# Optimization experiments

Measured on AMD Instinct MI355X. Metric: run time of the kernel, lower is better.

Reference implementation:

```python
import jax, jax.numpy as jnp
import numpy as np
import math

SQRT32 = math.sqrt(32.0)


def _l2norm(x, eps=1e-12):
    # matches torch.nn.functional.normalize(dim=-1): x / max(||x||, eps)
    n = jnp.linalg.norm(x, axis=-1, keepdims=True)
    return x / jnp.maximum(n, eps)


def setup_inputs() -> dict:
    key = jax.random.key(0)
    k1, k2 = jax.random.split(key)
    z = jax.random.normal(k1, (8, 256, 32, 32), dtype=jnp.float32)
    # trunc_normal_(std=0.02) init approximated by scaled normal
    embed_weight = jax.random.normal(k2, (16384, 256), dtype=jnp.float32) * 0.02
    return {"z": z, "embed_weight": embed_weight}


def reference(z, embed_weight):
    # z: [b, d, h, w] channel-first -> pack to [b*h*w, d]
    b, d, h, w = z.shape
    zf = jnp.transpose(z, (0, 2, 3, 1)).reshape(-1, d)  # [N, d]

    # l2_norm=True, no predefined codebook: distance = -z @ normalize(E)^T
    ew = _l2norm(embed_weight)                          # [K, d]
    dist = -(zf @ ew.T)                                 # [N, K]
    min_encoding_indices = jnp.argmin(dist, axis=1)     # [N]

    # gather UNnormalized embedding rows, then normalize (as in source)
    z_q = _l2norm(embed_weight[min_encoding_indices])   # [N, d]

    # straight-through estimator
    z_q = zf + jax.lax.stop_gradient(z_q - zf)

    loss = jnp.zeros((1,), dtype=z.dtype)

    # unpack to [b, h, w, d]
    zq_bhwd = z_q.reshape(b, h, w, d)
    # torch .long() truncates toward zero; astype(int) does the same
    bit_indices = (zq_bhwd * SQRT32).astype(jnp.int32) + 4
    zq_out = jnp.transpose(zq_bhwd, (0, 3, 1, 2))       # [b, d, h, w]

    return zq_out, min_encoding_indices, bit_indices, loss
```

## Files before the change

### kernel.cpp

```cpp
#include <hip/hip_runtime.h>
#include <math.h>

#define D      256
#define K      16384
#define NPTS   8192
#define DELTA  0.2f
#define LCAP   1024
#define MAXCAP 4000000u

#define O_IDX  2097152
#define O_BIT  2105344
#define O_LOSS 4202496

typedef __attribute__((ext_vector_type(8))) short bf16x8;
typedef __attribute__((ext_vector_type(4))) float f32x4;
typedef unsigned long long u64;

__device__ __forceinline__ unsigned f2s(float f) {
    unsigned u = __float_as_uint(f);
    return (u & 0x80000000u) ? ~u : (u | 0x80000000u);
}
__device__ __forceinline__ float s2f(unsigned s) {
    return __uint_as_float((s & 0x80000000u) ? (s & 0x7fffffffu) : ~s);
}
__device__ __forceinline__ unsigned short f2bf(float f) {
    unsigned u = __float_as_uint(f);
    u += 0x7fffu + ((u >> 16) & 1u);
    return (unsigned short)(u >> 16);
}


__global__ __launch_bounds__(256) void prep(const float* __restrict__ E,
                                            const float* __restrict__ z,
                                            float* __restrict__ den,
                                            unsigned short* __restrict__ ewbT,
                                            unsigned short* __restrict__ zfbT,
                                            float* __restrict__ zf32,
                                            unsigned* __restrict__ gmax,
                                            u64* __restrict__ keys,
                                            unsigned* __restrict__ cnt) {
    const int blk = blockIdx.x, tid = threadIdx.x;
    if (blk < 512) {
        const int lane = tid & 63, wave = tid >> 6;
        if (blk < 32)        gmax[blk * 256 + tid] = 0u;
        else if (blk < 64)   keys[(blk - 32) * 256 + tid] = 0ull;
        else if (blk == 64 && tid < 2) cnt[tid] = 0u;
        #pragma unroll
        for (int j = 0; j < 8; ++j) {
            const int row = blk * 32 + wave * 8 + j;
            const float4 v = *(const float4*)(E + (size_t)row * D + lane * 4);
            float ss = v.x * v.x + v.y * v.y + v.z * v.z + v.w * v.w;
            #pragma unroll
            for (int o = 1; o < 64; o <<= 1) ss += __shfl_xor(ss, o);
            const float dn = fmaxf(sqrtf(ss), 1e-12f);
            const unsigned lo = (unsigned)f2bf(v.x / dn) | ((unsigned)f2bf(v.y / dn) << 16);
            const unsigned hi = (unsigned)f2bf(v.z / dn) | ((unsigned)f2bf(v.w / dn) << 16);
            *(uint2*)(ewbT + ((size_t)(lane >> 1) * K + row) * 8 + (lane & 1) * 4)
                = make_uint2(lo, hi);
            if (lane == 0) den[row] = dn;
        }
    } else {
        const int bi = blk - 512;
        const int b = bi >> 4, hw0 = (bi & 15) * 64;
        __shared__ float t[64][65];
        for (int dc = 0; dc < D; dc += 64) {
            #pragma unroll
            for (int it = 0; it < 16; ++it) {
                const int idx = it * 256 + tid;
                const int dl = idx >> 6, hw = idx & 63;
                t[dl][hw] = z[(size_t)(b * 256 + dc + dl) * 1024 + hw0 + hw];
            }
            __syncthreads();
            #pragma unroll
            for (int it = 0; it < 16; ++it) {
                const int idx = it * 256 + tid;
                const int pl = idx >> 6, dl = idx & 63;
                const float v = t[dl][pl];
                const int p = b * 1024 + hw0 + pl, k = dc + dl;
                zfbT[((size_t)(k >> 3) * NPTS + p) * 8 + (k & 7)] = f2bf(v);
                zf32[(size_t)p * D + k] = v;
            }
            __syncthreads();
        }
    }
}

#define GEMM_CORE()                                                                 \
    f32x4 acc[4][4];                                                                \
    _Pragma("unroll")                                                               \
    for (int i = 0; i < 4; ++i)                                                     \
        _Pragma("unroll")                                                           \
        for (int j = 0; j < 4; ++j) acc[i][j] = (f32x4){0.f, 0.f, 0.f, 0.f};        \
    {                                                                               \
        const unsigned short* pA = zfbT + ((size_t)quad * NPTS + m0 + wm * 64 + col) * 8; \
        const unsigned short* pB = ewbT + ((size_t)quad * K    + n0 + wn * 64 + col) * 8; \
        _Pragma("unroll")                                                           \
        for (int dc = 0; dc < 8; ++dc) {                                            \
            bf16x8 af[4], bfr[4];                                                   \
            _Pragma("unroll")                                                       \
            for (int mt = 0; mt < 4; ++mt)                                          \
                af[mt] = *(const bf16x8*)(pA + (size_t)dc * 4 * NPTS * 8 + mt * 128);\
            _Pragma("unroll")                                                       \
            for (int nt = 0; nt < 4; ++nt)                                          \
                bfr[nt] = *(const bf16x8*)(pB + (size_t)dc * 4 * K * 8 + nt * 128); \
            _Pragma("unroll")                                                       \
            for (int mt = 0; mt < 4; ++mt)                                          \
                _Pragma("unroll")                                                   \
                for (int nt = 0; nt < 4; ++nt)                                      \
                    acc[mt][nt] = __builtin_amdgcn_mfma_f32_16x16x32_bf16(af[mt], bfr[nt], \
                                                                          acc[mt][nt], 0, 0, 0); \
        }                                                                           \
    }

__global__ __launch_bounds__(256, 3) void score_seed(const unsigned short* __restrict__ zfbT,
                                                     const unsigned short* __restrict__ ewbT,
                                                     unsigned* __restrict__ gmax,
                                                     u64* __restrict__ cand,
                                                     unsigned* __restrict__ cnt,
                                                     unsigned cap) {
    __shared__ unsigned thrS[128];
    __shared__ u64 lbuf[LCAP];
    __shared__ unsigned lcount, lbase;

    const int tid = threadIdx.x, lane = tid & 63, wave = tid >> 6;
    const int quad = lane >> 4, col = lane & 15;
    const int wm = wave >> 1, wn = wave & 1;
    const int m0 = blockIdx.x * 128;
    const int n0 = blockIdx.y * 128;
    const int shsrc = lane & 48;

    if (tid < 128) thrS[tid] = 0u;
    if (tid == 0) lcount = 0u;

    GEMM_CORE()
    __syncthreads();

    float red[4][4];
    #pragma unroll
    for (int mt = 0; mt < 4; ++mt)
        #pragma unroll
        for (int r = 0; r < 4; ++r)
            red[mt][r] = fmaxf(fmaxf(acc[mt][0][r], acc[mt][1][r]),
                               fmaxf(acc[mt][2][r], acc[mt][3][r]));
    #pragma unroll
    for (int off = 1; off < 16; off <<= 1)
        #pragma unroll
        for (int mt = 0; mt < 4; ++mt)
            #pragma unroll
            for (int r = 0; r < 4; ++r)
                red[mt][r] = fmaxf(red[mt][r], __shfl_xor(red[mt][r], off));
    #pragma unroll
    for (int mt = 0; mt < 4; ++mt)
        #pragma unroll
        for (int r = 0; r < 4; ++r) {
            const int pl = wm * 64 + mt * 16 + quad * 4 + r;
            unsigned cur = 0;
            if (col == 0) {
                const unsigned enc = f2s(red[mt][r]);
                const unsigned old = atomicMax(&thrS[pl], enc);
                cur = old > enc ? old : enc;
            }
            cur = (unsigned)__shfl((int)cur, shsrc);
            red[mt][r] = s2f(cur) - DELTA;
        }

    const int ncode0 = n0 + wn * 64 + col;
    #pragma unroll
    for (int mt = 0; mt < 4; ++mt) {
        #pragma unroll
        for (int r = 0; r < 4; ++r) {
            const float tp = red[mt][r];
            const unsigned pt = m0 + wm * 64 + mt * 16 + quad * 4 + r;
            #pragma unroll
            for (int nt = 0; nt < 4; ++nt) {
                const float v = acc[mt][nt][r];
                if (v >= tp) {
                    const unsigned slot = atomicAdd(&lcount, 1u);
                    const u64 e = ((u64)((pt << 14) | (unsigned)(ncode0 + nt * 16)) << 32)
                                  | f2s(v);
                    if (slot < LCAP) lbuf[slot] = e;
                    else {
                        const unsigned g = atomicAdd(cnt, 1u);
                        if (g < cap) cand[g] = e;
                    }
                }
            }
        }
    }

    __syncthreads();
    if (tid < 128) atomicMax(&gmax[m0 + tid], thrS[tid]);
    const unsigned m_ = lcount < LCAP ? lcount : LCAP;
    if (tid == 0) lbase = atomicAdd(cnt, m_);
    __syncthreads();
    for (unsigned i = tid; i < m_; i += 256) {
        const unsigned g = lbase + i;
        if (g < cap) cand[g] = lbuf[i];
    }
}

__global__ __launch_bounds__(256, 3) void score_main(const unsigned short* __restrict__ zfbT,
                                                     const unsigned short* __restrict__ ewbT,
                                                     const unsigned* __restrict__ gmax,
                                                     u64* __restrict__ cand,
                                                     unsigned* __restrict__ cnt,
                                                     unsigned cap) {
    __shared__ float thrL[128];
    __shared__ u64 lbuf[LCAP];
    __shared__ unsigned lcount, lbase;

    const int tid = threadIdx.x, lane = tid & 63, wave = tid >> 6;
    const int quad = lane >> 4, col = lane & 15;
    const int wm = wave >> 1, wn = wave & 1;
    const int m0 = blockIdx.x * 128;
    const int n0 = (16 + blockIdx.y) * 128;

    if (tid < 128) thrL[tid] = s2f(gmax[m0 + tid]) - DELTA;
    if (tid == 0) lcount = 0u;

    GEMM_CORE()
    __syncthreads();

    const int ncode0 = n0 + wn * 64 + col;
    #pragma unroll
    for (int mt = 0; mt < 4; ++mt) {
        #pragma unroll
        for (int r = 0; r < 4; ++r) {
            const int pl = wm * 64 + mt * 16 + quad * 4 + r;
            const float tp = thrL[pl];
            #pragma unroll
            for (int nt = 0; nt < 4; ++nt) {
                const float v = acc[mt][nt][r];
                if (v >= tp) {
                    const unsigned slot = atomicAdd(&lcount, 1u);
                    const u64 e = ((u64)(((unsigned)pl + m0) << 14 | (unsigned)(ncode0 + nt * 16)) << 32)
                                  | f2s(v);
                    if (slot < LCAP) lbuf[slot] = e;
                    else {
                        const unsigned g = atomicAdd(cnt, 1u);
                        if (g < cap) cand[g] = e;
                    }
                }
            }
        }
    }

    __syncthreads();
    const unsigned m_ = lcount < LCAP ? lcount : LCAP;
    if (tid == 0) lbase = atomicAdd(cnt, m_);
    __syncthreads();
    for (unsigned i = tid; i < m_; i += 256) {
        const unsigned g = lbase + i;
        if (g < cap) cand[g] = lbuf[i];
    }
}

__global__ __launch_bounds__(256) void cand_max(const u64* __restrict__ cand,
                                                const unsigned* __restrict__ cnt,
                                                unsigned* __restrict__ gmax,
                                                unsigned cap) {
    const unsigned total = min(cnt[0], cap);
    const unsigned stride = gridDim.x * 256;
    for (unsigned i = blockIdx.x * 256 + threadIdx.x; i < total; i += stride) {
        const u64 e = cand[i];
        atomicMax(&gmax[(unsigned)(e >> 46)], (unsigned)(e & 0xffffffffull));
    }
}

__global__ __launch_bounds__(256) void rescore(const float* __restrict__ zf32,
                                               const float* __restrict__ E,
                                               const float* __restrict__ den,
                                               const unsigned* __restrict__ gmax,
                                               const u64* __restrict__ cand,
                                               const unsigned* __restrict__ cnt,
                                               u64* __restrict__ keys,
                                               unsigned cap) {
    const unsigned total = min(cnt[0], cap);
    const int lane = threadIdx.x & 63;
    const unsigned w = (blockIdx.x * 256 + threadIdx.x) >> 6;
    const unsigned nw = gridDim.x * 4;
    for (unsigned base = w * 64; base < total; base += nw * 64) {
        const unsigned i = base + lane;
        u64 e = 0;
        bool keep = false;
        if (i < total) {
            e = cand[i];
            const int p = (int)(e >> 46);
            keep = (s2f((unsigned)(e & 0xffffffffull)) >= s2f(gmax[p]) - DELTA);
        }
        u64 mask = __ballot(keep);
        while (mask) {
            const int src = __ffsll((long long)mask) - 1;
            mask &= mask - 1;
            const unsigned pc = (unsigned)__shfl((int)(unsigned)(e >> 32), src);
            const int p = pc >> 14, c = pc & 16383;
            const float dinv = 1.0f / den[c];
            const float4 a = *(const float4*)(zf32 + (size_t)p * D + lane * 4);
            const float4 b = *(const float4*)(E + (size_t)c * D + lane * 4);
            float sv = fmaf(a.x, b.x * dinv, fmaf(a.y, b.y * dinv,
                       fmaf(a.z, b.z * dinv, a.w * (b.w * dinv))));
            #pragma unroll
            for (int o = 1; o < 64; o <<= 1) sv += __shfl_xor(sv, o);
            if (lane == 0)
                atomicMax(keys + p, ((u64)f2s(sv) << 32) | (unsigned)(16383 - c));
        }
    }
}

__global__ __launch_bounds__(256) void finalize(const float* __restrict__ E,
                                                const float* __restrict__ den,
                                                const u64* __restrict__ keys,
                                                float* __restrict__ out) {
    __shared__ float t[32][257];
    __shared__ int sIdx[32];
    __shared__ float sDen[32];
    const int tid = threadIdx.x;
    const int n0 = blockIdx.x * 32;
    if (tid < 32) {
        const u64 key = keys[n0 + tid];
        const int idx = 16383 - (int)(unsigned)(key & 0xffffffffull);
        sIdx[tid] = idx;
        sDen[tid] = den[idx];
        out[O_IDX + n0 + tid] = (float)idx;
    }
    __syncthreads();
    const float S = 5.65685424949238019520675489683895f;
    #pragma unroll 4
    for (int i = 0; i < 32; ++i) {
        const float v = E[(size_t)sIdx[i] * D + tid] / sDen[i];
        t[i][tid] = v;
        out[O_BIT + (size_t)(n0 + i) * D + tid] = (float)((int)(v * S) + 4);
    }
    __syncthreads();
    const int b = n0 >> 10, hw0 = n0 & 1023;
    const int hwl = tid & 31, cg = tid >> 5;
    #pragma unroll 4
    for (int cc = 0; cc < 32; ++cc) {
        const int c = cc * 8 + cg;
        out[(size_t)(b * 256 + c) * 1024 + hw0 + hwl] = t[hwl][c];
    }
    if (n0 == 0 && tid == 0) out[O_LOSS] = 0.0f;
}

extern "C" void kernel_launch(void* const* d_in, const int* in_sizes, int n_in,
                              void* d_out, int out_size, void* d_ws, size_t ws_size,
                              hipStream_t stream) {
    const float* z = (const float*)d_in[0];
    const float* E = (const float*)d_in[1];
    float* out = (float*)d_out;

    char* w = (char*)d_ws;
    unsigned short* ewbT = (unsigned short*)w;  w += (size_t)K * D * 2;
    unsigned short* zfbT = (unsigned short*)w;  w += (size_t)NPTS * D * 2;
    float*          zf32 = (float*)w;           w += (size_t)NPTS * D * 4;
    u64*            keys = (u64*)w;             w += (size_t)NPTS * 8;
    float*          den  = (float*)w;           w += (size_t)K * 4;
    unsigned*       gmax = (unsigned*)w;        w += (size_t)NPTS * 4;
    unsigned*       cnt  = (unsigned*)w;        w += 256;
    u64*            cand = (u64*)w;
    const size_t fixed = (size_t)(w - (char*)d_ws);
    const size_t avail = ws_size > fixed ? (ws_size - fixed) / 8 : 0;
    const unsigned cap = (unsigned)(avail < (size_t)MAXCAP ? avail : (size_t)MAXCAP);

    prep<<<640, 256, 0, stream>>>(E, z, den, ewbT, zfbT, zf32, gmax, keys, cnt);

    dim3 gpre(NPTS / 128, 16);
    score_seed<<<gpre, 256, 0, stream>>>(zfbT, ewbT, gmax, cand, cnt, cap);
    dim3 gmain(NPTS / 128, 112);
    score_main<<<gmain, 256, 0, stream>>>(zfbT, ewbT, gmax, cand, cnt, cap);

    cand_max<<<256, 256, 0, stream>>>(cand, cnt, gmax, cap);
    rescore<<<1024, 256, 0, stream>>>(zf32, E, den, gmax, cand, cnt, keys, cap);
    finalize<<<NPTS / 32, 256, 0, stream>>>(E, den, keys, out);
}
```

Baseline: 265.6 us.

## Keep A fragments in registers and loop over codebook sub-tiles per block

The score kernels now use 512-thread blocks that load each block's 128-point A fragments into registers once. Each block then loops over eight 128-code sub-tiles, reusing A and amortizing the candidate buffer flush, with a larger shared candidate buffer. The seed kernel tightens its per-point threshold progressively across sub-tiles. The cost is far fewer blocks (64 seed, 960 main) and higher register pressure, which may cut parallelism and latency hiding on the seed pass.

```diff
diff --git a/kernel.cpp b/kernel.cpp
--- a/kernel.cpp
+++ b/kernel.cpp
@@ -5,7 +5,7 @@
 #define K      16384
 #define NPTS   8192
 #define DELTA  0.2f
-#define LCAP   1024
+#define LCAP   4096
 #define MAXCAP 4000000u
 
 #define O_IDX  2097152
@@ -85,34 +85,82 @@
     }
 }
 
-#define GEMM_CORE()                                                                 \
-    f32x4 acc[4][4];                                                                \
+
+#define SCORE_PROLOG()                                                              \
+    const int tid = threadIdx.x, lane = tid & 63, wave = tid >> 6;                  \
+    const int quad = lane >> 4, col = lane & 15;                                    \
+    const int wm = wave & 3, wn = wave >> 2;                                        \
+    const int m0 = blockIdx.x * 128;                                                \
+    const int shsrc = lane & 48;                                                    \
+    (void)shsrc;                                                                    \
+    bf16x8 af[2][8];                                                                \
+    {                                                                               \
+        const unsigned short* pA = zfbT + ((size_t)quad * NPTS + m0 + wm * 32 + col) * 8; \
+        _Pragma("unroll")                                                           \
+        for (int mt = 0; mt < 2; ++mt)                                              \
+            _Pragma("unroll")                                                       \
+            for (int dc = 0; dc < 8; ++dc)                                          \
+                af[mt][dc] = *(const bf16x8*)(pA + ((size_t)dc * 4 * NPTS + mt * 16) * 8); \
+    }
+
+#define SUB_GEMM(N0S)                                                               \
+    f32x4 acc[2][4];                                                                \
     _Pragma("unroll")                                                               \
-    for (int i = 0; i < 4; ++i)                                                     \
+    for (int i = 0; i < 2; ++i)                                                     \
         _Pragma("unroll")                                                           \
         for (int j = 0; j < 4; ++j) acc[i][j] = (f32x4){0.f, 0.f, 0.f, 0.f};        \
     {                                                                               \
-        const unsigned short* pA = zfbT + ((size_t)quad * NPTS + m0 + wm * 64 + col) * 8; \
-        const unsigned short* pB = ewbT + ((size_t)quad * K    + n0 + wn * 64 + col) * 8; \
-        _Pragma("unroll")                                                           \
-        for (int dc = 0; dc < 8; ++dc) {                                            \
-            bf16x8 af[4], bfr[4];                                                   \
-            _Pragma("unroll")                                                       \
-            for (int mt = 0; mt < 4; ++mt)                                          \
-                af[mt] = *(const bf16x8*)(pA + (size_t)dc * 4 * NPTS * 8 + mt * 128);\
+        const unsigned short* pB = ewbT + ((size_t)quad * K + (N0S) + wn * 64 + col) * 8; \
+        bf16x8 bfr[8][4];                                                           \
+        _Pragma("unroll")                                                           \
+        for (int dc = 0; dc < 8; ++dc)                                              \
             _Pragma("unroll")                                                       \
             for (int nt = 0; nt < 4; ++nt)                                          \
-                bfr[nt] = *(const bf16x8*)(pB + (size_t)dc * 4 * K * 8 + nt * 128); \
+                bfr[dc][nt] = *(const bf16x8*)(pB + ((size_t)dc * 4 * K + nt * 16) * 8); \
+        _Pragma("unroll")                                                           \
+        for (int dc = 0; dc < 8; ++dc)                                              \
             _Pragma("unroll")                                                       \
-            for (int mt = 0; mt < 4; ++mt)                                          \
+            for (int mt = 0; mt < 2; ++mt)                                          \
                 _Pragma("unroll")                                                   \
                 for (int nt = 0; nt < 4; ++nt)                                      \
-                    acc[mt][nt] = __builtin_amdgcn_mfma_f32_16x16x32_bf16(af[mt], bfr[nt], \
+                    acc[mt][nt] = __builtin_amdgcn_mfma_f32_16x16x32_bf16(af[mt][dc], bfr[dc][nt], \
                                                                           acc[mt][nt], 0, 0, 0); \
+    }
+
+#define APPEND_CANDS(N0S, THR2D)                                                    \
+    _Pragma("unroll")                                                               \
+    for (int mt = 0; mt < 2; ++mt) {                                                \
+        _Pragma("unroll")                                                           \
+        for (int r = 0; r < 4; ++r) {                                               \
+            const float tp = THR2D[mt][r];                                          \
+            const unsigned pt = m0 + wm * 32 + mt * 16 + quad * 4 + r;              \
+            _Pragma("unroll")                                                       \
+            for (int nt = 0; nt < 4; ++nt) {                                        \
+                const float v = acc[mt][nt][r];                                     \
+                if (v >= tp) {                                                      \
+                    const unsigned slot = atomicAdd(&lcount, 1u);                   \
+                    const unsigned code = (N0S) + wn * 64 + nt * 16 + col;          \
+                    const u64 e = ((u64)((pt << 14) | code) << 32) | f2s(v);        \
+                    if (slot < LCAP) lbuf[slot] = e;                                \
+                    else {                                                          \
+                        const unsigned g = atomicAdd(cnt, 1u);                      \
+                        if (g < cap) cand[g] = e;                                   \
+                    }                                                               \
+                }                                                                   \
+            }                                                                       \
         }                                                                           \
     }
 
-__global__ __launch_bounds__(256, 3) void score_seed(const unsigned short* __restrict__ zfbT,
+#define FLUSH_LBUF()                                                                \
+    const unsigned m_ = lcount < LCAP ? lcount : LCAP;                              \
+    if (tid == 0) lbase = atomicAdd(cnt, m_);                                       \
+    __syncthreads();                                                                \
+    for (unsigned i = tid; i < m_; i += 512) {                                      \
+        const unsigned g = lbase + i;                                               \
+        if (g < cap) cand[g] = lbuf[i];                                             \
+    }
+
+__global__ __launch_bounds__(512, 2) void score_seed(const unsigned short* __restrict__ zfbT,
                                                      const unsigned short* __restrict__ ewbT,
                                                      unsigned* __restrict__ gmax,
                                                      u64* __restrict__ cand,
@@ -122,84 +170,51 @@
     __shared__ u64 lbuf[LCAP];
     __shared__ unsigned lcount, lbase;
 
-    const int tid = threadIdx.x, lane = tid & 63, wave = tid >> 6;
-    const int quad = lane >> 4, col = lane & 15;
-    const int wm = wave >> 1, wn = wave & 1;
-    const int m0 = blockIdx.x * 128;
-    const int n0 = blockIdx.y * 128;
-    const int shsrc = lane & 48;
-
+    SCORE_PROLOG()
     if (tid < 128) thrS[tid] = 0u;
     if (tid == 0) lcount = 0u;
-
-    GEMM_CORE()
-    __syncthreads();
-
-    float red[4][4];
-    #pragma unroll
-    for (int mt = 0; mt < 4; ++mt)
-        #pragma unroll
-        for (int r = 0; r < 4; ++r)
-            red[mt][r] = fmaxf(fmaxf(acc[mt][0][r], acc[mt][1][r]),
-                               fmaxf(acc[mt][2][r], acc[mt][3][r]));
-    #pragma unroll
-    for (int off = 1; off < 16; off <<= 1)
-        #pragma unroll
-        for (int mt = 0; mt < 4; ++mt)
+    __syncthreads();
+
+    for (int sub = 0; sub < 8; ++sub) {
+        const int n0s = sub * 128;
+        SUB_GEMM(n0s)
+
+        float red[2][4], thr[2][4];
+        #pragma unroll
+        for (int mt = 0; mt < 2; ++mt)
             #pragma unroll
             for (int r = 0; r < 4; ++r)
-                red[mt][r] = fmaxf(red[mt][r], __shfl_xor(red[mt][r], off));
-    #pragma unroll
-    for (int mt = 0; mt < 4; ++mt)
-        #pragma unroll
-        for (int r = 0; r < 4; ++r) {
-            const int pl = wm * 64 + mt * 16 + quad * 4 + r;
-            unsigned cur = 0;
-            if (col == 0) {
-                const unsigned enc = f2s(red[mt][r]);
-                const unsigned old = atomicMax(&thrS[pl], enc);
-                cur = old > enc ? old : enc;
+                red[mt][r] = fmaxf(fmaxf(acc[mt][0][r], acc[mt][1][r]),
+                                   fmaxf(acc[mt][2][r], acc[mt][3][r]));
+        #pragma unroll
+        for (int off = 1; off < 16; off <<= 1)
+            #pragma unroll
+            for (int mt = 0; mt < 2; ++mt)
+                #pragma unroll
+                for (int r = 0; r < 4; ++r)
+                    red[mt][r] = fmaxf(red[mt][r], __shfl_xor(red[mt][r], off));
+        #pragma unroll
+        for (int mt = 0; mt < 2; ++mt)
+            #pragma unroll
+            for (int r = 0; r < 4; ++r) {
+                unsigned cur = 0;
+                if (col == 0) {
+                    const unsigned enc = f2s(red[mt][r]);
+                    const unsigned old = atomicMax(&thrS[wm * 32 + mt * 16 + quad * 4 + r], enc);
+                    cur = old > enc ? old : enc;
+                }
+                cur = (unsigned)__shfl((int)cur, shsrc);
+                thr[mt][r] = s2f(cur) - DELTA;
             }
-            cur = (unsigned)__shfl((int)cur, shsrc);
-            red[mt][r] = s2f(cur) - DELTA;
-        }
-
-    const int ncode0 = n0 + wn * 64 + col;
-    #pragma unroll
-    for (int mt = 0; mt < 4; ++mt) {
-        #pragma unroll
-        for (int r = 0; r < 4; ++r) {
-            const float tp = red[mt][r];
-            const unsigned pt = m0 + wm * 64 + mt * 16 + quad * 4 + r;
-            #pragma unroll
-            for (int nt = 0; nt < 4; ++nt) {
-                const float v = acc[mt][nt][r];
-                if (v >= tp) {
-                    const unsigned slot = atomicAdd(&lcount, 1u);
-                    const u64 e = ((u64)((pt << 14) | (unsigned)(ncode0 + nt * 16)) << 32)
-                                  | f2s(v);
-                    if (slot < LCAP) lbuf[slot] = e;
-                    else {
-                        const unsigned g = atomicAdd(cnt, 1u);
-                        if (g < cap) cand[g] = e;
-                    }
-                }
-            }
-        }
+        APPEND_CANDS(n0s, thr)
     }
 
     __syncthreads();
     if (tid < 128) atomicMax(&gmax[m0 + tid], thrS[tid]);
-    const unsigned m_ = lcount < LCAP ? lcount : LCAP;
-    if (tid == 0) lbase = atomicAdd(cnt, m_);
-    __syncthreads();
-    for (unsigned i = tid; i < m_; i += 256) {
-        const unsigned g = lbase + i;
-        if (g < cap) cand[g] = lbuf[i];
-    }
-}
-
-__global__ __launch_bounds__(256, 3) void score_main(const unsigned short* __restrict__ zfbT,
+    FLUSH_LBUF()
+}
+
+__global__ __launch_bounds__(512, 2) void score_main(const unsigned short* __restrict__ zfbT,
                                                      const unsigned short* __restrict__ ewbT,
                                                      const unsigned* __restrict__ gmax,
                                                      u64* __restrict__ cand,
@@ -209,50 +224,27 @@
     __shared__ u64 lbuf[LCAP];
     __shared__ unsigned lcount, lbase;
 
-    const int tid = threadIdx.x, lane = tid & 63, wave = tid >> 6;
-    const int quad = lane >> 4, col = lane & 15;
-    const int wm = wave >> 1, wn = wave & 1;
-    const int m0 = blockIdx.x * 128;
-    const int n0 = (16 + blockIdx.y) * 128;
-
+    SCORE_PROLOG()
+    const int nbase = 1024 + blockIdx.y * 1024;
     if (tid < 128) thrL[tid] = s2f(gmax[m0 + tid]) - DELTA;
     if (tid == 0) lcount = 0u;
-
-    GEMM_CORE()
-    __syncthreads();
-
-    const int ncode0 = n0 + wn * 64 + col;
+    __syncthreads();
+
+    float thr[2][4];
     #pragma unroll
-    for (int mt = 0; mt < 4; ++mt) {
-        #pragma unroll
-        for (int r = 0; r < 4; ++r) {
-            const int pl = wm * 64 + mt * 16 + quad * 4 + r;
-            const float tp = thrL[pl];
-            #pragma unroll
-            for (int nt = 0; nt < 4; ++nt) {
-                const float v = acc[mt][nt][r];
-                if (v >= tp) {
-                    const unsigned slot = atomicAdd(&lcount, 1u);
-                    const u64 e = ((u64)(((unsigned)pl + m0) << 14 | (unsigned)(ncode0 + nt * 16)) << 32)
-                                  | f2s(v);
-                    if (slot < LCAP) lbuf[slot] = e;
-                    else {
-                        const unsigned g = atomicAdd(cnt, 1u);
-                        if (g < cap) cand[g] = e;
-                    }
-                }
-            }
-        }
-    }
-
-    __syncthreads();
-    const unsigned m_ = lcount < LCAP ? lcount : LCAP;
-    if (tid == 0) lbase = atomicAdd(cnt, m_);
-    __syncthreads();
-    for (unsigned i = tid; i < m_; i += 256) {
-        const unsigned g = lbase + i;
-        if (g < cap) cand[g] = lbuf[i];
-    }
+    for (int mt = 0; mt < 2; ++mt)
+        #pragma unroll
+        for (int r = 0; r < 4; ++r)
+            thr[mt][r] = thrL[wm * 32 + mt * 16 + quad * 4 + r];
+
+    for (int sub = 0; sub < 8; ++sub) {
+        const int n0s = nbase + sub * 128;
+        SUB_GEMM(n0s)
+        APPEND_CANDS(n0s, thr)
+    }
+
+    __syncthreads();
+    FLUSH_LBUF()
 }
 
 __global__ __launch_bounds__(256) void cand_max(const u64* __restrict__ cand,
@@ -364,10 +356,9 @@
 
     prep<<<640, 256, 0, stream>>>(E, z, den, ewbT, zfbT, zf32, gmax, keys, cnt);
 
-    dim3 gpre(NPTS / 128, 16);
-    score_seed<<<gpre, 256, 0, stream>>>(zfbT, ewbT, gmax, cand, cnt, cap);
-    dim3 gmain(NPTS / 128, 112);
-    score_main<<<gmain, 256, 0, stream>>>(zfbT, ewbT, gmax, cand, cnt, cap);
+    score_seed<<<64, 512, 0, stream>>>(zfbT, ewbT, gmax, cand, cnt, cap);
+    dim3 gmain(64, 15);
+    score_main<<<gmain, 512, 0, stream>>>(zfbT, ewbT, gmax, cand, cnt, cap);
 
     cand_max<<<256, 256, 0, stream>>>(cand, cnt, gmax, cap);
     rescore<<<1024, 256, 0, stream>>>(zf32, E, den, gmax, cand, cnt, keys, cap);
```

New measurement: 280.6 us. 5.6% more time.
